# Optimization experiments

Measured on AMD Instinct MI355X. Metric: run time of the kernel, lower is better.

Reference implementation:

```python
import jax, jax.numpy as jnp
import numpy as np

N_NODES = 100000
N_EDGES = 3200000
IN_FEAT = 128
OUT_FEAT = 128
NUM_RELS = 16
NUM_BASES = 8


def setup_inputs() -> dict:
    key = jax.random.key(0)
    ks = jax.random.split(key, 7)
    x = jax.random.normal(ks[0], (N_NODES, IN_FEAT), dtype=jnp.float32)
    src = jax.random.randint(ks[1], (N_EDGES,), 0, N_NODES, dtype=jnp.int64)
    dst = jax.random.randint(ks[2], (N_EDGES,), 0, N_NODES, dtype=jnp.int64)
    etypes = jax.random.randint(ks[3], (N_EDGES,), 0, NUM_RELS, dtype=jnp.int64)
    # xavier_uniform with gain for relu = sqrt(2)
    gain = float(np.sqrt(2.0))
    limit_w = gain * float(np.sqrt(6.0 / (IN_FEAT + OUT_FEAT)))
    weight = jax.random.uniform(ks[4], (NUM_BASES, IN_FEAT, OUT_FEAT), dtype=jnp.float32,
                                minval=-limit_w, maxval=limit_w)
    limit_c = float(np.sqrt(6.0 / (NUM_RELS + NUM_BASES)))
    w_comp = jax.random.uniform(ks[5], (NUM_RELS, NUM_BASES), dtype=jnp.float32,
                                minval=-limit_c, maxval=limit_c)
    h_bias = jnp.zeros((OUT_FEAT,), dtype=jnp.float32)
    return {"x": x, "weight": weight, "w_comp": w_comp, "h_bias": h_bias,
            "src": src, "dst": dst, "etypes": etypes}


def reference(x, weight, w_comp, h_bias, src, dst, etypes):
    # basis decomposition: per-relation weight [R, in, out]
    W = jnp.einsum('rb,bio->rio', w_comp, weight)
    # transform all nodes under every relation: h[r, n, o]
    h = jnp.einsum('ni,rio->rno', x, W)
    # per-edge message = transformed source feature under the edge's relation type
    msg = h[etypes, src]  # [E, out]
    # scatter-sum messages into destination nodes
    node_repr = jax.ops.segment_sum(msg, dst, num_segments=N_NODES)
    node_repr = node_repr + h_bias
    return node_repr
```

## Files before the change

kernel.cpp:

```cpp
#include <hip/hip_runtime.h>
#include <hip/hip_bf16.h>
#include <stdint.h>

#define N_NODES   100000
#define N_EDGES   3200000
#define IN_FEAT   128
#define OUT_FEAT  128
#define NUM_RELS  16
#define NUM_BASES 8
#define M_PAD     100096
#define NBKT      391
#define NB        512

using short8 = __attribute__((ext_vector_type(8))) short;
using v4f    = __attribute__((ext_vector_type(4))) float;

__device__ inline unsigned short f2bf_rne(float f) {
    __hip_bfloat16 h = __float2bfloat16(f);
    return *reinterpret_cast<unsigned short*>(&h);
}
__device__ inline float bf2f(unsigned short u) {
    union { uint32_t i; float f; } x;
    x.i = ((uint32_t)u) << 16;
    return x.f;
}

__global__ void conv_x(const float* __restrict__ x, unsigned short* __restrict__ xb) {
    int id = blockIdx.x * 256 + threadIdx.x;
    int base = id * 4;
    ushort4 o;
    if (base < N_NODES * IN_FEAT) {
        const float4 v = reinterpret_cast<const float4*>(x)[id];
        o.x = f2bf_rne(v.x); o.y = f2bf_rne(v.y);
        o.z = f2bf_rne(v.z); o.w = f2bf_rne(v.w);
    } else {
        o.x = o.y = o.z = o.w = 0;
    }
    reinterpret_cast<ushort4*>(xb)[id] = o;
}

__global__ void build_ut(const float* __restrict__ weight,
                         unsigned short* __restrict__ Ut) {
    int id = blockIdx.x * 256 + threadIdx.x;
    int o  = id >> 10;
    int kk = id & 1023;
    int b  = kk >> 7;
    int i  = kk & 127;
    Ut[id] = f2bf_rne(weight[(b * IN_FEAT + i) * OUT_FEAT + o]);
}

__global__ __launch_bounds__(512) void coarse_hist(const int* __restrict__ dst,
                                                   int* __restrict__ histG,
                                                   int nbuck) {
    extern __shared__ int lh[];
    for (int i = threadIdx.x; i < nbuck; i += 512) lh[i] = 0;
    __syncthreads();
    const int NG = N_EDGES / 4;
    const int stride = NB * 512;
    for (int g = blockIdx.x * 512 + threadIdx.x; g < NG; g += stride) {
        const int4 d4 = reinterpret_cast<const int4*>(dst)[g];
        atomicAdd(&lh[d4.x >> 8], 1);
        atomicAdd(&lh[d4.y >> 8], 1);
        atomicAdd(&lh[d4.z >> 8], 1);
        atomicAdd(&lh[d4.w >> 8], 1);
    }
    __syncthreads();
    for (int i = threadIdx.x; i < nbuck; i += 512)
        histG[i * NB + blockIdx.x] = lh[i];
}

__global__ void scan_part(const int* __restrict__ data, int* __restrict__ partial, int K) {
    __shared__ int sh[256];
    const int tid = threadIdx.x, b = blockIdx.x;
    const int i0 = b * 4096 + tid * 16;
    int s = 0;
#pragma unroll
    for (int k = 0; k < 16; ++k) { int i = i0 + k; if (i < K) s += data[i]; }
    sh[tid] = s;
    __syncthreads();
    for (int st = 128; st > 0; st >>= 1) {
        if (tid < st) sh[tid] += sh[tid + st];
        __syncthreads();
    }
    if (tid == 0) partial[b] = sh[0];
}

__global__ __launch_bounds__(512) void scan_mid(int* __restrict__ partial, int G) {
    __shared__ int sh[512];
    const int tid = threadIdx.x;
    int v = (tid < G) ? partial[tid] : 0;
    sh[tid] = v;
    __syncthreads();
    for (int st = 1; st < 512; st <<= 1) {
        int t = (tid >= st) ? sh[tid - st] : 0;
        __syncthreads();
        sh[tid] += t;
        __syncthreads();
    }
    if (tid < G) partial[tid] = sh[tid] - v;
}

__global__ void scan_final(int* __restrict__ data, const int* __restrict__ partial, int K) {
    __shared__ int sh[256];
    const int tid = threadIdx.x, b = blockIdx.x;
    const int i0 = b * 4096 + tid * 16;
    int s = 0;
#pragma unroll
    for (int k = 0; k < 16; ++k) { int i = i0 + k; if (i < K) s += data[i]; }
    sh[tid] = s;
    __syncthreads();
    for (int st = 1; st < 256; st <<= 1) {
        int t = (tid >= st) ? sh[tid - st] : 0;
        __syncthreads();
        sh[tid] += t;
        __syncthreads();
    }
    int run = partial[b] + sh[tid] - s;
#pragma unroll
    for (int k = 0; k < 16; ++k) {
        int i = i0 + k;
        if (i < K) {
            int c = data[i];
            data[i] = run;
            run += c;
        }
    }
}

__global__ __launch_bounds__(512) void coarse_place(const int* __restrict__ src,
                                                    const int* __restrict__ dst,
                                                    const int* __restrict__ et,
                                                    const int* __restrict__ histS,
                                                    int* __restrict__ entries,
                                                    int nbuck) {
    extern __shared__ int cur[];
    for (int i = threadIdx.x; i < nbuck; i += 512)
        cur[i] = histS[i * NB + blockIdx.x];
    __syncthreads();
    const int NG = N_EDGES / 4;
    const int stride = NB * 512;
    for (int g = blockIdx.x * 512 + threadIdx.x; g < NG; g += stride) {
        const int4 s4 = reinterpret_cast<const int4*>(src)[g];
        const int4 d4 = reinterpret_cast<const int4*>(dst)[g];
        const int4 t4 = reinterpret_cast<const int4*>(et)[g];
        int p0 = atomicAdd(&cur[d4.x >> 8], 1);
        int p1 = atomicAdd(&cur[d4.y >> 8], 1);
        int p2 = atomicAdd(&cur[d4.z >> 8], 1);
        int p3 = atomicAdd(&cur[d4.w >> 8], 1);
        entries[p0] = ((d4.x & 255) << 21) | ((t4.x & 15) << 17) | s4.x;
        entries[p1] = ((d4.y & 255) << 21) | ((t4.y & 15) << 17) | s4.y;
        entries[p2] = ((d4.z & 255) << 21) | ((t4.z & 15) << 17) | s4.z;
        entries[p3] = ((d4.w & 255) << 21) | ((t4.w & 15) << 17) | s4.w;
    }
}

__global__ __launch_bounds__(256) void fine_sort(const int* __restrict__ entries,
                                                 const int* __restrict__ histS,
                                                 int* __restrict__ perm,
                                                 int* __restrict__ off,
                                                 int nbuck) {
    __shared__ int cnt[4096];
    __shared__ int bs[256];
    const int tid = threadIdx.x, b = blockIdx.x;
    const int start = histS[b * NB];
    const int end   = (b + 1 < nbuck) ? histS[(b + 1) * NB] : N_EDGES;

#pragma unroll
    for (int k = 0; k < 16; ++k) cnt[tid * 16 + k] = 0;
    __syncthreads();
    for (int i = start + tid; i < end; i += 256)
        atomicAdd(&cnt[entries[i] >> 17], 1);
    __syncthreads();

    int c[16];
    int tsum = 0;
#pragma unroll
    for (int k = 0; k < 16; ++k) { c[k] = cnt[tid * 16 + k]; tsum += c[k]; }
    bs[tid] = tsum;
    __syncthreads();
    for (int st = 1; st < 256; st <<= 1) {
        int t = (tid >= st) ? bs[tid - st] : 0;
        __syncthreads();
        bs[tid] += t;
        __syncthreads();
    }
    const int excl = bs[tid] - tsum;

    const int d = b * 256 + tid;
    if (d < N_NODES) off[d] = start + excl;
    if (b == nbuck - 1 && tid == 0) off[N_NODES] = N_EDGES;

    int run = excl;
#pragma unroll
    for (int k = 0; k < 16; ++k) { cnt[tid * 16 + k] = run; run += c[k]; }
    __syncthreads();
    for (int i = start + tid; i < end; i += 256) {
        int en = entries[i];
        int p = atomicAdd(&cnt[en >> 17], 1);
        perm[start + p] = en & 0x1FFFFF;
    }
}

__global__ void gather_z(const int* __restrict__ off, const int* __restrict__ perm,
                         const unsigned short* __restrict__ xb,
                         const float* __restrict__ w_comp,
                         unsigned short* __restrict__ zb) {
    __shared__ float csh[NUM_RELS * NUM_BASES];
    if (threadIdx.x < NUM_RELS * NUM_BASES) csh[threadIdx.x] = w_comp[threadIdx.x];
    __syncthreads();
    const int d = blockIdx.x * 4 + (threadIdx.x >> 6);
    const int lane = threadIdx.x & 63;
    float2 z[8];
#pragma unroll
    for (int b = 0; b < 8; ++b) z[b] = make_float2(0.f, 0.f);

    if (d < N_NODES) {
        const int e0 = off[d], e1 = off[d + 1];
        const unsigned short* xl = xb + lane * 2;
        int cur = -1;
        float2 srun = make_float2(0.f, 0.f);

        auto flush = [&]() {
            const float4 cA = *reinterpret_cast<const float4*>(&csh[cur * 8]);
            const float4 cB = *reinterpret_cast<const float4*>(&csh[cur * 8 + 4]);
            z[0].x += cA.x * srun.x; z[0].y += cA.x * srun.y;
            z[1].x += cA.y * srun.x; z[1].y += cA.y * srun.y;
            z[2].x += cA.z * srun.x; z[2].y += cA.z * srun.y;
            z[3].x += cA.w * srun.x; z[3].y += cA.w * srun.y;
            z[4].x += cB.x * srun.x; z[4].y += cB.x * srun.y;
            z[5].x += cB.y * srun.x; z[5].y += cB.y * srun.y;
            z[6].x += cB.z * srun.x; z[6].y += cB.z * srun.y;
            z[7].x += cB.w * srun.x; z[7].y += cB.w * srun.y;
        };
        auto step = [&](int p, ushort2 v) {
            int rl = p >> 17;
            if (rl != cur) {
                flush();
                cur = rl;
                srun = make_float2(0.f, 0.f);
            }
            srun.x += bf2f(v.x);
            srun.y += bf2f(v.y);
        };

        if (e0 < e1) {
            cur = perm[e0] >> 17;
            int e = e0;
            for (; e + 8 <= e1; e += 8) {
                int p[8];
#pragma unroll
                for (int j = 0; j < 8; ++j) p[j] = perm[e + j];
                ushort2 v[8];
#pragma unroll
                for (int j = 0; j < 8; ++j)
                    v[j] = *reinterpret_cast<const ushort2*>(
                        xl + (size_t)(p[j] & 0x1FFFF) * 128);
#pragma unroll
                for (int j = 0; j < 8; ++j) step(p[j], v[j]);
            }
            for (; e < e1; ++e) {
                int p = perm[e];
                ushort2 v = *reinterpret_cast<const ushort2*>(
                    xl + (size_t)(p & 0x1FFFF) * 128);
                step(p, v);
            }
            flush();
        }
    }

    unsigned short* zr = zb + (size_t)d * 1024 + lane * 2;
#pragma unroll
    for (int b = 0; b < 8; ++b) {
        unsigned int u = (unsigned int)f2bf_rne(z[b].x)
                       | ((unsigned int)f2bf_rne(z[b].y) << 16);
        __builtin_nontemporal_store(u, reinterpret_cast<unsigned int*>(zr + b * 128));
    }
}

__global__ __launch_bounds__(256, 2) void zgemm(const unsigned short* __restrict__ zb,
                                                const unsigned short* __restrict__ Ut,
                                                const float* __restrict__ bias,
                                                float* __restrict__ out) {
    __shared__ unsigned short lA[128 * 128];
    __shared__ unsigned short lB[128 * 128];

    const int mb = blockIdx.x;
    const int tid  = threadIdx.x;
    const int wid  = tid >> 6;
    const int lane = tid & 63;
    const int wm = wid >> 1, wn = wid & 1;
    const int ml = lane & 15, kgrp = lane >> 4;

    const unsigned short* gA = zb + (size_t)mb * 128 * 1024;

    v4f acc[4][4];
#pragma unroll
    for (int i = 0; i < 4; ++i)
#pragma unroll
        for (int j = 0; j < 4; ++j)
            acc[i][j] = (v4f){0.f, 0.f, 0.f, 0.f};

    for (int kt = 0; kt < 8; ++kt) {
#pragma unroll
        for (int it = 0; it < 8; ++it) {
            int sbase = it * 256 + wid * 64;
            int s = sbase + lane;
            int row = s >> 4;
            int cc = (s & 15) ^ (row & 15);
            __builtin_amdgcn_global_load_lds(
                (const __attribute__((address_space(1))) void*)(gA + (size_t)row * 1024 + kt * 128 + cc * 8),
                (__attribute__((address_space(3))) void*)(&lA[sbase * 8]), 16, 0, 0);
            __builtin_amdgcn_global_load_lds(
                (const __attribute__((address_space(1))) void*)(Ut + (size_t)row * 1024 + kt * 128 + cc * 8),
                (__attribute__((address_space(3))) void*)(&lB[sbase * 8]), 16, 0, 0);
        }
        __syncthreads();

#pragma unroll
        for (int kb = 0; kb < 4; ++kb) {
            const int cc = kb * 4 + kgrp;
            short8 af[4], bfr[4];
#pragma unroll
            for (int tm = 0; tm < 4; ++tm) {
                int rA = wm * 64 + tm * 16 + ml;
                af[tm] = *reinterpret_cast<const short8*>(&lA[(rA * 16 + (cc ^ (rA & 15))) * 8]);
            }
#pragma unroll
            for (int tn = 0; tn < 4; ++tn) {
                int rB = wn * 64 + tn * 16 + ml;
                bfr[tn] = *reinterpret_cast<const short8*>(&lB[(rB * 16 + (cc ^ (rB & 15))) * 8]);
            }
#pragma unroll
            for (int tm = 0; tm < 4; ++tm)
#pragma unroll
                for (int tn = 0; tn < 4; ++tn)
                    acc[tm][tn] = __builtin_amdgcn_mfma_f32_16x16x32_bf16(af[tm], bfr[tn], acc[tm][tn], 0, 0, 0);
        }
        __syncthreads();
    }

    const int row0 = mb * 128 + wm * 64;
    const int col0 = wn * 64;
#pragma unroll
    for (int tm = 0; tm < 4; ++tm)
#pragma unroll
        for (int rr = 0; rr < 4; ++rr) {
            int row = row0 + tm * 16 + kgrp * 4 + rr;
            if (row < N_NODES) {
                size_t rb = (size_t)row * OUT_FEAT;
#pragma unroll
                for (int tn = 0; tn < 4; ++tn) {
                    int col = col0 + tn * 16 + ml;
                    out[rb + col] = acc[tm][tn][rr] + bias[col];
                }
            }
        }
}

static inline size_t align256(size_t a) { return (a + 255) & ~(size_t)255; }

extern "C" void kernel_launch(void* const* d_in, const int* in_sizes, int n_in,
                              void* d_out, int out_size, void* d_ws, size_t ws_size,
                              hipStream_t stream) {
    const float* x      = (const float*)d_in[0];
    const float* weight = (const float*)d_in[1];
    const float* w_comp = (const float*)d_in[2];
    const float* h_bias = (const float*)d_in[3];
    const int*   src    = (const int*)d_in[4];
    const int*   dst    = (const int*)d_in[5];
    const int*   etypes = (const int*)d_in[6];
    float* out = (float*)d_out;

    const int nbuck = NBKT;
    const int K2 = nbuck * NB;
    const int G2 = (K2 + 4095) / 4096;

    size_t a = 512 * 1024;
    size_t xb_o = a;   a = align256(a + (size_t)M_PAD * 128 * 2);
    size_t perm_o = a; a = align256(a + (size_t)N_EDGES * 4);
    size_t off_o = a;  a = align256(a + ((size_t)N_NODES + 1) * 4);
    size_t part_o = a; a = align256(a + 512 * 4);
    size_t zb_o = a;

    char* w = (char*)d_ws;
    unsigned short* Ut      = (unsigned short*)(w);
    unsigned short* xb      = (unsigned short*)(w + xb_o);
    int*            perm    = (int*)(w + perm_o);
    int*            off     = (int*)(w + off_o);
    int*            partial = (int*)(w + part_o);
    unsigned short* zb      = (unsigned short*)(w + zb_o);
    int*            entries = (int*)(w + zb_o);
    int*            histG   = (int*)(w + zb_o + 13 * 1024 * 1024);

    conv_x<<<12512, 256, 0, stream>>>(x, xb);
    build_ut<<<512, 256, 0, stream>>>(weight, Ut);

    coarse_hist<<<NB, 512, nbuck * 4, stream>>>(dst, histG, nbuck);
    scan_part<<<G2, 256, 0, stream>>>(histG, partial, K2);
    scan_mid<<<1, 512, 0, stream>>>(partial, G2);
    scan_final<<<G2, 256, 0, stream>>>(histG, partial, K2);
    coarse_place<<<NB, 512, nbuck * 4, stream>>>(src, dst, etypes, histG, entries, nbuck);
    fine_sort<<<nbuck, 256, 0, stream>>>(entries, histG, perm, off, nbuck);

    gather_z<<<25024, 256, 0, stream>>>(off, perm, xb, w_comp, zb);
    zgemm<<<782, 256, 0, stream>>>(zb, Ut, h_bias, out);
}
```

Before: 415.3 us.

## Fuse gather of basis-projected features with the GEMM through shared memory

Merges the gather_z and zgemm kernels into one kernel. Each 512-thread block gathers 16 destination nodes into an LDS tile of per-basis aggregated bf16 features, then runs 16x16x32 MFMAs against Ut read straight from global memory. This removes the write and re-read of the ~200MB zb intermediate and one kernel launch. In exchange the GEMM has tiny M tiles with no LDS reuse of Ut, so every block re-reads all of Ut (mostly from cache), and the MFMA phase is serialized behind the latency-bound gather inside each block.

```diff
diff --git a/kernel.cpp b/kernel.cpp
--- a/kernel.cpp
+++ b/kernel.cpp
@@ -11,6 +11,7 @@
 #define M_PAD     100096
 #define NBKT      391
 #define NB        512
+#define ZROW      1032
 
 using short8 = __attribute__((ext_vector_type(8))) short;
 using v4f    = __attribute__((ext_vector_type(4))) float;
@@ -201,160 +202,111 @@
     }
 }
 
-__global__ void gather_z(const int* __restrict__ off, const int* __restrict__ perm,
-                         const unsigned short* __restrict__ xb,
-                         const float* __restrict__ w_comp,
-                         unsigned short* __restrict__ zb) {
-    __shared__ float csh[NUM_RELS * NUM_BASES];
-    if (threadIdx.x < NUM_RELS * NUM_BASES) csh[threadIdx.x] = w_comp[threadIdx.x];
-    __syncthreads();
-    const int d = blockIdx.x * 4 + (threadIdx.x >> 6);
-    const int lane = threadIdx.x & 63;
-    float2 z[8];
-#pragma unroll
-    for (int b = 0; b < 8; ++b) z[b] = make_float2(0.f, 0.f);
-
-    if (d < N_NODES) {
-        const int e0 = off[d], e1 = off[d + 1];
-        const unsigned short* xl = xb + lane * 2;
-        int cur = -1;
-        float2 srun = make_float2(0.f, 0.f);
-
-        auto flush = [&]() {
-            const float4 cA = *reinterpret_cast<const float4*>(&csh[cur * 8]);
-            const float4 cB = *reinterpret_cast<const float4*>(&csh[cur * 8 + 4]);
-            z[0].x += cA.x * srun.x; z[0].y += cA.x * srun.y;
-            z[1].x += cA.y * srun.x; z[1].y += cA.y * srun.y;
-            z[2].x += cA.z * srun.x; z[2].y += cA.z * srun.y;
-            z[3].x += cA.w * srun.x; z[3].y += cA.w * srun.y;
-            z[4].x += cB.x * srun.x; z[4].y += cB.x * srun.y;
-            z[5].x += cB.y * srun.x; z[5].y += cB.y * srun.y;
-            z[6].x += cB.z * srun.x; z[6].y += cB.z * srun.y;
-            z[7].x += cB.w * srun.x; z[7].y += cB.w * srun.y;
-        };
-        auto step = [&](int p, ushort2 v) {
-            int rl = p >> 17;
-            if (rl != cur) {
-                flush();
-                cur = rl;
-                srun = make_float2(0.f, 0.f);
-            }
-            srun.x += bf2f(v.x);
-            srun.y += bf2f(v.y);
-        };
-
-        if (e0 < e1) {
-            cur = perm[e0] >> 17;
-            int e = e0;
-            for (; e + 8 <= e1; e += 8) {
-                int p[8];
-#pragma unroll
-                for (int j = 0; j < 8; ++j) p[j] = perm[e + j];
-                ushort2 v[8];
-#pragma unroll
-                for (int j = 0; j < 8; ++j)
-                    v[j] = *reinterpret_cast<const ushort2*>(
-                        xl + (size_t)(p[j] & 0x1FFFF) * 128);
-#pragma unroll
-                for (int j = 0; j < 8; ++j) step(p[j], v[j]);
-            }
-            for (; e < e1; ++e) {
-                int p = perm[e];
-                ushort2 v = *reinterpret_cast<const ushort2*>(
-                    xl + (size_t)(p & 0x1FFFF) * 128);
-                step(p, v);
-            }
-            flush();
-        }
-    }
-
-    unsigned short* zr = zb + (size_t)d * 1024 + lane * 2;
-#pragma unroll
-    for (int b = 0; b < 8; ++b) {
-        unsigned int u = (unsigned int)f2bf_rne(z[b].x)
-                       | ((unsigned int)f2bf_rne(z[b].y) << 16);
-        __builtin_nontemporal_store(u, reinterpret_cast<unsigned int*>(zr + b * 128));
-    }
-}
-
-__global__ __launch_bounds__(256, 2) void zgemm(const unsigned short* __restrict__ zb,
+__global__ __launch_bounds__(512) void fused_gz(const int* __restrict__ off,
+                                                const int* __restrict__ perm,
+                                                const unsigned short* __restrict__ xb,
+                                                const float* __restrict__ w_comp,
                                                 const unsigned short* __restrict__ Ut,
                                                 const float* __restrict__ bias,
                                                 float* __restrict__ out) {
-    __shared__ unsigned short lA[128 * 128];
-    __shared__ unsigned short lB[128 * 128];
-
-    const int mb = blockIdx.x;
-    const int tid  = threadIdx.x;
-    const int wid  = tid >> 6;
-    const int lane = tid & 63;
-    const int wm = wid >> 1, wn = wid & 1;
-    const int ml = lane & 15, kgrp = lane >> 4;
-
-    const unsigned short* gA = zb + (size_t)mb * 128 * 1024;
-
-    v4f acc[4][4];
-#pragma unroll
-    for (int i = 0; i < 4; ++i)
-#pragma unroll
-        for (int j = 0; j < 4; ++j)
-            acc[i][j] = (v4f){0.f, 0.f, 0.f, 0.f};
-
-    for (int kt = 0; kt < 8; ++kt) {
-#pragma unroll
-        for (int it = 0; it < 8; ++it) {
-            int sbase = it * 256 + wid * 64;
-            int s = sbase + lane;
-            int row = s >> 4;
-            int cc = (s & 15) ^ (row & 15);
-            __builtin_amdgcn_global_load_lds(
-                (const __attribute__((address_space(1))) void*)(gA + (size_t)row * 1024 + kt * 128 + cc * 8),
-                (__attribute__((address_space(3))) void*)(&lA[sbase * 8]), 16, 0, 0);
-            __builtin_amdgcn_global_load_lds(
-                (const __attribute__((address_space(1))) void*)(Ut + (size_t)row * 1024 + kt * 128 + cc * 8),
-                (__attribute__((address_space(3))) void*)(&lB[sbase * 8]), 16, 0, 0);
-        }
-        __syncthreads();
-
-#pragma unroll
-        for (int kb = 0; kb < 4; ++kb) {
-            const int cc = kb * 4 + kgrp;
-            short8 af[4], bfr[4];
-#pragma unroll
-            for (int tm = 0; tm < 4; ++tm) {
-                int rA = wm * 64 + tm * 16 + ml;
-                af[tm] = *reinterpret_cast<const short8*>(&lA[(rA * 16 + (cc ^ (rA & 15))) * 8]);
-            }
-#pragma unroll
-            for (int tn = 0; tn < 4; ++tn) {
-                int rB = wn * 64 + tn * 16 + ml;
-                bfr[tn] = *reinterpret_cast<const short8*>(&lB[(rB * 16 + (cc ^ (rB & 15))) * 8]);
-            }
-#pragma unroll
-            for (int tm = 0; tm < 4; ++tm)
-#pragma unroll
-                for (int tn = 0; tn < 4; ++tn)
-                    acc[tm][tn] = __builtin_amdgcn_mfma_f32_16x16x32_bf16(af[tm], bfr[tn], acc[tm][tn], 0, 0, 0);
-        }
-        __syncthreads();
-    }
-
-    const int row0 = mb * 128 + wm * 64;
-    const int col0 = wn * 64;
-#pragma unroll
-    for (int tm = 0; tm < 4; ++tm)
-#pragma unroll
-        for (int rr = 0; rr < 4; ++rr) {
-            int row = row0 + tm * 16 + kgrp * 4 + rr;
-            if (row < N_NODES) {
-                size_t rb = (size_t)row * OUT_FEAT;
-#pragma unroll
-                for (int tn = 0; tn < 4; ++tn) {
-                    int col = col0 + tn * 16 + ml;
-                    out[rb + col] = acc[tm][tn][rr] + bias[col];
+    __shared__ unsigned short zt[16 * ZROW];
+    __shared__ float csh[NUM_RELS * NUM_BASES];
+    if (threadIdx.x < NUM_RELS * NUM_BASES) csh[threadIdx.x] = w_comp[threadIdx.x];
+    __syncthreads();
+
+    const int wid  = threadIdx.x >> 6;
+    const int lane = threadIdx.x & 63;
+    const int nbase = blockIdx.x * 16;
+
+    for (int i = 0; i < 2; ++i) {
+        const int lr = wid * 2 + i;
+        const int d  = nbase + lr;
+        float2 z[8];
+#pragma unroll
+        for (int b = 0; b < 8; ++b) z[b] = make_float2(0.f, 0.f);
+
+        if (d < N_NODES) {
+            const int e0 = off[d], e1 = off[d + 1];
+            const unsigned short* xl = xb + lane * 2;
+            int cur = -1;
+            float2 srun = make_float2(0.f, 0.f);
+
+            auto flush = [&]() {
+                const float4 cA = *reinterpret_cast<const float4*>(&csh[cur * 8]);
+                const float4 cB = *reinterpret_cast<const float4*>(&csh[cur * 8 + 4]);
+                z[0].x += cA.x * srun.x; z[0].y += cA.x * srun.y;
+                z[1].x += cA.y * srun.x; z[1].y += cA.y * srun.y;
+                z[2].x += cA.z * srun.x; z[2].y += cA.z * srun.y;
+                z[3].x += cA.w * srun.x; z[3].y += cA.w * srun.y;
+                z[4].x += cB.x * srun.x; z[4].y += cB.x * srun.y;
+                z[5].x += cB.y * srun.x; z[5].y += cB.y * srun.y;
+                z[6].x += cB.z * srun.x; z[6].y += cB.z * srun.y;
+                z[7].x += cB.w * srun.x; z[7].y += cB.w * srun.y;
+            };
+            auto step = [&](int p, ushort2 v) {
+                int rl = p >> 17;
+                if (rl != cur) {
+                    flush();
+                    cur = rl;
+                    srun = make_float2(0.f, 0.f);
                 }
+                srun.x += bf2f(v.x);
+                srun.y += bf2f(v.y);
+            };
+
+            if (e0 < e1) {
+                cur = perm[e0] >> 17;
+                int e = e0;
+                for (; e + 8 <= e1; e += 8) {
+                    int p[8];
+#pragma unroll
+                    for (int j = 0; j < 8; ++j) p[j] = perm[e + j];
+                    ushort2 v[8];
+#pragma unroll
+                    for (int j = 0; j < 8; ++j)
+                        v[j] = *reinterpret_cast<const ushort2*>(
+                            xl + (size_t)(p[j] & 0x1FFFF) * 128);
+#pragma unroll
+                    for (int j = 0; j < 8; ++j) step(p[j], v[j]);
+                }
+                for (; e < e1; ++e) {
+                    int p = perm[e];
+                    ushort2 v = *reinterpret_cast<const ushort2*>(
+                        xl + (size_t)(p & 0x1FFFF) * 128);
+                    step(p, v);
+                }
+                flush();
             }
         }
+
+        unsigned short* zr = &zt[lr * ZROW + lane * 2];
+#pragma unroll
+        for (int b = 0; b < 8; ++b) {
+            unsigned int u = (unsigned int)f2bf_rne(z[b].x)
+                           | ((unsigned int)f2bf_rne(z[b].y) << 16);
+            *reinterpret_cast<unsigned int*>(zr + b * 128) = u;
+        }
+    }
+    __syncthreads();
+
+    const int ml = lane & 15, kg = lane >> 4;
+    const int col0 = wid * 16;
+    v4f acc = (v4f){0.f, 0.f, 0.f, 0.f};
+    const unsigned short* gB = Ut + (size_t)(col0 + ml) * 1024 + kg * 8;
+#pragma unroll 4
+    for (int kt = 0; kt < 32; ++kt) {
+        short8 af = *reinterpret_cast<const short8*>(&zt[ml * ZROW + kt * 32 + kg * 8]);
+        short8 bf = *reinterpret_cast<const short8*>(gB + kt * 32);
+        acc = __builtin_amdgcn_mfma_f32_16x16x32_bf16(af, bf, acc, 0, 0, 0);
+    }
+
+    const float bv = bias[col0 + ml];
+#pragma unroll
+    for (int rr = 0; rr < 4; ++rr) {
+        int row = nbase + kg * 4 + rr;
+        if (row < N_NODES)
+            out[(size_t)row * OUT_FEAT + col0 + ml] = acc[rr] + bv;
+    }
 }
 
 static inline size_t align256(size_t a) { return (a + 255) & ~(size_t)255; }
@@ -380,7 +332,8 @@
     size_t perm_o = a; a = align256(a + (size_t)N_EDGES * 4);
     size_t off_o = a;  a = align256(a + ((size_t)N_NODES + 1) * 4);
     size_t part_o = a; a = align256(a + 512 * 4);
-    size_t zb_o = a;
+    size_t ent_o = a;  a = align256(a + (size_t)N_EDGES * 4);
+    size_t hist_o = a; a = align256(a + (size_t)K2 * 4);
 
     char* w = (char*)d_ws;
     unsigned short* Ut      = (unsigned short*)(w);
@@ -388,9 +341,8 @@
     int*            perm    = (int*)(w + perm_o);
     int*            off     = (int*)(w + off_o);
     int*            partial = (int*)(w + part_o);
-    unsigned short* zb      = (unsigned short*)(w + zb_o);
-    int*            entries = (int*)(w + zb_o);
-    int*            histG   = (int*)(w + zb_o + 13 * 1024 * 1024);
+    int*            entries = (int*)(w + ent_o);
+    int*            histG   = (int*)(w + hist_o);
 
     conv_x<<<12512, 256, 0, stream>>>(x, xb);
     build_ut<<<512, 256, 0, stream>>>(weight, Ut);
@@ -402,6 +354,5 @@
     coarse_place<<<NB, 512, nbuck * 4, stream>>>(src, dst, etypes, histG, entries, nbuck);
     fine_sort<<<nbuck, 256, 0, stream>>>(entries, histG, perm, off, nbuck);
 
-    gather_z<<<25024, 256, 0, stream>>>(off, perm, xb, w_comp, zb);
-    zgemm<<<782, 256, 0, stream>>>(zb, Ut, h_bias, out);
-}
+    fused_gz<<<M_PAD / 16, 512, 0, stream>>>(off, perm, xb, w_comp, Ut, h_bias, out);
+}
```

After: 494.5 us. 19.1% more time.
